# Kernel tuning notes

Hardware: AMD Instinct MI355X
Metric: run time of the kernel (lower is better)

The kernel has to match this reference:

```python
import math
import jax, jax.numpy as jnp
import numpy as np

B, IMG, P, D, DEPTH, NH, HD = 8, 384, 16, 768, 12, 12, 64
NREG, NS, NF = 4, 5, 16            # registers, special tokens (1 cls + 4 reg), rope freqs
HP = IMG // P                      # 24 patches per side
NPATCH = HP * HP                   # 576
ROPE_DIM = 2 * NF                  # 32
SCALE = HD ** -0.5


def setup_inputs() -> dict:
    key = jax.random.key(0)
    ks = jax.random.split(key, 12)
    s = 0.02
    rn = lambda k, shape: (jax.random.normal(k, shape, jnp.float32) * s)
    L, DF = DEPTH, 4 * D
    inp = {
        "pixel_values": jax.random.normal(ks[0], (B, 3, IMG, IMG), jnp.float32),
        "conv_w": rn(ks[1], (D, 3, P, P)),
        "conv_b": jnp.zeros((D,), jnp.float32),
        "cls_token": rn(ks[2], (1, 1, D)),
        "storage_tokens": rn(ks[3], (1, NREG, D)),
        "periods": jnp.exp(jnp.linspace(0.0, math.log(100.0), NF)).astype(jnp.float32),
        "ln1_s": jnp.ones((L, D), jnp.float32),
        "ln1_b": jnp.zeros((L, D), jnp.float32),
        "qkv_w": rn(ks[4], (L, 3 * D, D)),
        "qkv_b": rn(ks[5], (L, 3 * D)),
        "bias_mask": jnp.zeros((L, 3 * D), jnp.float32),  # buffer init zeros -> bias nulled
        "proj_w": rn(ks[6], (L, D, D)),
        "proj_b": jnp.zeros((L, D), jnp.float32),
        "ls1": jnp.ones((L, D), jnp.float32),
        "ln2_s": jnp.ones((L, D), jnp.float32),
        "ln2_b": jnp.zeros((L, D), jnp.float32),
        "fc1_w": rn(ks[7], (L, DF, D)),
        "fc1_b": jnp.zeros((L, DF), jnp.float32),
        "fc2_w": rn(ks[8], (L, D, DF)),
        "fc2_b": jnp.zeros((L, D), jnp.float32),
        "ls2": jnp.ones((L, D), jnp.float32),
        "lnf_s": jnp.ones((D,), jnp.float32),
        "lnf_b": jnp.zeros((D,), jnp.float32),
    }
    return inp


def _ln(x, s, b):
    mu = x.mean(-1, keepdims=True)
    var = ((x - mu) ** 2).mean(-1, keepdims=True)
    return (x - mu) / jnp.sqrt(var + 1e-6) * s + b


def _rot(x, cos, sin):
    # x: [b, h, n_patch, 2*NF]; cos/sin: [n_patch, NF]; interleaved even/odd rotation
    even, odd = x[..., 0::2], x[..., 1::2]
    return jnp.stack([even * cos - odd * sin, even * sin + odd * cos], axis=-1).reshape(x.shape)


def _forward(pixel_values, conv_w, conv_b, cls_token, storage_tokens, periods,
             ln1_s, ln1_b, qkv_w, qkv_b, bias_mask, proj_w, proj_b, ls1,
             ln2_s, ln2_b, fc1_w, fc1_b, fc2_w, fc2_b, ls2, lnf_s, lnf_b):
    b = pixel_values.shape[0]
    # Patch embed: stride == kernel conv as reshape + einsum
    xp = pixel_values.reshape(b, 3, HP, P, HP, P)
    tok = jnp.einsum('bchpwq,dcpq->bhwd', xp, conv_w) + conv_b       # [b,HP,HP,D]
    tok = tok.reshape(b, NPATCH, D)
    x = jnp.concatenate([jnp.broadcast_to(cls_token, (b, 1, D)),
                         jnp.broadcast_to(storage_tokens, (b, NREG, D)), tok], axis=1)
    n = x.shape[1]

    # RoPE tables (periods buffer; freqs = 2*pi / periods)
    freqs = (2.0 * math.pi) / periods                                 # [NF]
    pos = jnp.arange(HP, dtype=jnp.float32)
    gy, gx = jnp.meshgrid(pos, pos, indexing='ij')
    ax = gx.reshape(-1, 1) * freqs                                    # [NPATCH, NF]
    ay = gy.reshape(-1, 1) * freqs
    cos_x, sin_x = jnp.cos(ax), jnp.sin(ax)
    cos_y, sin_y = jnp.cos(ay), jnp.sin(ay)

    def blk(h, p):
        (l1s, l1b, qw, qb, bm, pw, pb, g1, l2s, l2b, f1w, f1b, f2w, f2b, g2) = p
        h1 = _ln(h, l1s, l1b)
        qkv = h1 @ qw.T + qb * bm                                     # bias nulled by mask
        qkv = qkv.reshape(b, n, 3, NH, HD).transpose(2, 0, 3, 1, 4)   # [3,b,NH,n,HD]
        q, k, v = qkv[0], qkv[1], qkv[2]
        # rotary on patch tokens; rope_total == HD so the whole head is rotated
        qp, kp = q[:, :, NS:], k[:, :, NS:]
        qp = jnp.concatenate([_rot(qp[..., :ROPE_DIM], cos_x, sin_x),
                              _rot(qp[..., ROPE_DIM:], cos_y, sin_y)], axis=-1)
        kp = jnp.concatenate([_rot(kp[..., :ROPE_DIM], cos_x, sin_x),
                              _rot(kp[..., ROPE_DIM:], cos_y, sin_y)], axis=-1)
        q = jnp.concatenate([q[:, :, :NS], qp], axis=2)
        k = jnp.concatenate([k[:, :, :NS], kp], axis=2)
        attn = jax.nn.softmax(jnp.einsum('bhqd,bhkd->bhqk', q, k) * SCALE, axis=-1)
        o = jnp.einsum('bhqk,bhkd->bhqd', attn, v).transpose(0, 2, 1, 3).reshape(b, n, D)
        h = h + g1 * (o @ pw.T + pb)
        h2 = _ln(h, l2s, l2b)
        m = jax.nn.gelu(h2 @ f1w.T + f1b, approximate=False) @ f2w.T + f2b
        h = h + g2 * m
        return h, None

    params = (ln1_s, ln1_b, qkv_w, qkv_b, bias_mask, proj_w, proj_b, ls1,
              ln2_s, ln2_b, fc1_w, fc1_b, fc2_w, fc2_b, ls2)
    x, _ = jax.lax.scan(blk, x, params)
    return _ln(x, lnf_s, lnf_b)


def reference(pixel_values, conv_w, conv_b, cls_token, storage_tokens, periods,
              ln1_s, ln1_b, qkv_w, qkv_b, bias_mask, proj_w, proj_b, ls1,
              ln2_s, ln2_b, fc1_w, fc1_b, fc2_w, fc2_b, ls2, lnf_s, lnf_b):
    return _forward(pixel_values, conv_w, conv_b, cls_token, storage_tokens, periods,
                    ln1_s, ln1_b, qkv_w, qkv_b, bias_mask, proj_w, proj_b, ls1,
                    ln2_s, ln2_b, fc1_w, fc1_b, fc2_w, fc2_b, ls2, lnf_s, lnf_b)
```

## Files before the change

### kernel.cpp

```cpp
#include <hip/hip_runtime.h>
#include <math.h>

typedef unsigned short u16;
typedef __attribute__((ext_vector_type(8))) short bf8;
typedef __attribute__((ext_vector_type(4))) float f4;

#define DEV static __device__ __forceinline__

DEV u16 f2b(float f){
  unsigned u = __builtin_bit_cast(unsigned, f);
  u += 0x7fffu + ((u >> 16) & 1u);
  return (u16)(u >> 16);
}
DEV float b2f(u16 h){
  unsigned u = ((unsigned)h) << 16;
  return __builtin_bit_cast(float, u);
}

#define BATCH  8
#define NTOK   581
#define NPAD   640
#define DIM    768
#define DFF    3072
#define NHEAD  12
#define HDIM   64
#define NLAYER 12
#define MTOK   (BATCH*NTOK)
#define MPAD2  4736
#define MCONV  (BATCH*576)
#define ATTN_SCALE 0.125f
#define BHEADS (BATCH*NHEAD)
#define QSZ    ((long long)BHEADS*NPAD*HDIM)

enum { EPI_CONV=0, EPI_QKV, EPI_PROJ, EPI_GELU, EPI_FC2 };

DEV int xcdswz(int lin, int n){
  int q = n >> 3, r = n & 7;
  int x = lin & 7, o = lin >> 3;
  return (x < r ? x*(q+1) : r*(q+1) + (x - r)*q) + o;
}

template<int EPI, int BM>
__global__ __launch_bounds__(256) void gemmRS(
    const u16* __restrict__ A, int lda,
    const u16* __restrict__ B, int ldb, int K,
    const float* __restrict__ bias,
    const float* __restrict__ aux,
    float* __restrict__ Cf,
    u16* __restrict__ Cb)
{
  constexpr int MR = BM / 32;
  const int gx = gridDim.x;
  const int lin = blockIdx.y * gx + blockIdx.x;
  const int tix = xcdswz(lin, gx * gridDim.y);
  const int bm = (tix / gx) * BM, bn = (tix % gx) * 64;
  __shared__ __attribute__((aligned(16))) u16 As[2][BM][40];
  __shared__ __attribute__((aligned(16))) u16 Bs[2][64][40];
  const int tid  = threadIdx.x;
  const int lane = tid & 63, wid = tid >> 6;
  const int wr = wid >> 1, wc = wid & 1;
  const int srow = tid >> 2, scol = (tid & 3) * 8;
  const u16* gA0 = A + (long long)(bm + srow) * lda + scol;
  const u16* gA1 = A + (long long)(bm + 64 + srow) * lda + scol;
  const u16* gB  = B + (long long)(bn + srow) * ldb + scol;
  const int frow = lane & 15, quad = lane >> 4, fk = quad * 8;

  f4 acc[MR][2] = {};
  const int T = K >> 5;

  auto compute = [&](int buf){
    bf8 af[MR], bf[2];
    #pragma unroll
    for (int m = 0; m < MR; ++m)
      af[m] = *(const bf8*)&As[buf][wr*(BM/2) + m*16 + frow][fk];
    #pragma unroll
    for (int n = 0; n < 2; ++n)
      bf[n] = *(const bf8*)&Bs[buf][wc*32 + n*16 + frow][fk];
    #pragma unroll
    for (int m = 0; m < MR; ++m)
    #pragma unroll
    for (int n = 0; n < 2; ++n)
      acc[m][n] = __builtin_amdgcn_mfma_f32_16x16x32_bf16(af[m], bf[n], acc[m][n], 0, 0, 0);
  };

  bf8 xA0, xA1, xB, yA0, yA1, yB;
  xA0 = *(const bf8*)gA0;        if constexpr (BM == 128) xA1 = *(const bf8*)gA1;
  xB  = *(const bf8*)gB;
  yA0 = *(const bf8*)(gA0 + 32); if constexpr (BM == 128) yA1 = *(const bf8*)(gA1 + 32);
  yB  = *(const bf8*)(gB + 32);
  *(bf8*)&As[0][srow][scol] = xA0;
  if constexpr (BM == 128) *(bf8*)&As[0][64 + srow][scol] = xA1;
  *(bf8*)&Bs[0][srow][scol] = xB;
  __syncthreads();

  for (int t = 0; t < T; t += 2){
    if (t + 2 < T){
      xA0 = *(const bf8*)(gA0 + (t+2)*32);
      if constexpr (BM == 128) xA1 = *(const bf8*)(gA1 + (t+2)*32);
      xB  = *(const bf8*)(gB  + (t+2)*32);
    }
    *(bf8*)&As[1][srow][scol] = yA0;
    if constexpr (BM == 128) *(bf8*)&As[1][64 + srow][scol] = yA1;
    *(bf8*)&Bs[1][srow][scol] = yB;
    compute(0);
    __syncthreads();
    if (t + 3 < T){
      yA0 = *(const bf8*)(gA0 + (t+3)*32);
      if constexpr (BM == 128) yA1 = *(const bf8*)(gA1 + (t+3)*32);
      yB  = *(const bf8*)(gB  + (t+3)*32);
    }
    if (t + 2 < T){
      *(bf8*)&As[0][srow][scol] = xA0;
      if constexpr (BM == 128) *(bf8*)&As[0][64 + srow][scol] = xA1;
      *(bf8*)&Bs[0][srow][scol] = xB;
    }
    compute(1);
    __syncthreads();
  }

  #pragma unroll
  for (int mi = 0; mi < MR; ++mi)
  #pragma unroll
  for (int ni = 0; ni < 2; ++ni){
    f4 v = acc[mi][ni];
    int col = bn + wc*32 + ni*16 + frow;
    int r0  = bm + wr*(BM/2) + mi*16 + quad*4;
    #pragma unroll
    for (int j = 0; j < 4; ++j){
      int m = r0 + j;
      float val = v[j];
      if constexpr (EPI == EPI_CONV){
        int b = m / 576, p = m % 576;
        Cf[((long long)b*NTOK + 5 + p)*DIM + col] = val + bias[col];
      } else if constexpr (EPI == EPI_QKV){
        if (m < MTOK){
          int b = m / NTOK, t = m % NTOK;
          int which = col / DIM, rem = col % DIM;
          int h = rem / HDIM, hd = rem % HDIM;
          float x = val + bias[col];
          long long bh = (long long)(b*NHEAD + h);
          if (which == 0) x *= ATTN_SCALE;
          if (which == 2)
            Cb[2*QSZ + (bh*HDIM + hd)*NPAD + t] = f2b(x);
          else
            Cb[(long long)which*QSZ + (bh*NPAD + t)*HDIM + hd] = f2b(x);
        }
      } else if constexpr (EPI == EPI_PROJ || EPI == EPI_FC2){
        if (m < MTOK)
          Cf[(long long)m*DIM + col] += aux[col] * (val + bias[col]);
      } else if constexpr (EPI == EPI_GELU){
        float x = val + bias[col];
        float g = 0.5f * x * (1.0f + erff(x * 0.70710678118f));
        Cb[(long long)m*DFF + col] = f2b(g);
      }
    }
  }
}

__global__ __launch_bounds__(256) void flash_k(
    const u16* __restrict__ Q, const u16* __restrict__ K,
    const u16* __restrict__ VT, u16* __restrict__ obuf)
{
  const int lid = blockIdx.x;
  const int xcd = lid & 7, slot = lid >> 3;
  const int bh = xcd * 12 + slot / 10;
  const int qb = slot % 10;
  const int b = bh / NHEAD, h = bh % NHEAD;
  const int tid = threadIdx.x, lane = tid & 63, w = tid >> 6;
  const int frow = lane & 15, quad = lane >> 4;
  __shared__ u16 P[4][16][80];
  const u16* Qb = Q  + (long long)bh * NPAD * HDIM;
  const u16* Kb = K  + (long long)bh * NPAD * HDIM;
  const u16* Vb = VT + (long long)bh * HDIM * NPAD;
  const bf8 qa0 = *(const bf8*)&Qb[(qb*64 + w*16 + frow)*HDIM + quad*8];
  const bf8 qa1 = *(const bf8*)&Qb[(qb*64 + w*16 + frow)*HDIM + 32 + quad*8];
  f4 o[4] = {};
  float m[4], l[4];
  #pragma unroll
  for (int j = 0; j < 4; ++j){ m[j] = -1e30f; l[j] = 0.0f; }

  bf8 kb0[4], kb1[4];
  #pragma unroll
  for (int n = 0; n < 4; ++n){
    const u16* kr = &Kb[(n*16 + frow)*HDIM + quad*8];
    kb0[n] = *(const bf8*)kr;
    kb1[n] = *(const bf8*)(kr + 32);
  }

  for (int kt = 0; kt < NPAD/64; ++kt){
    bf8 vb0[4], vb1[4];
    #pragma unroll
    for (int n = 0; n < 4; ++n){
      const u16* vr = &Vb[(n*16 + frow)*NPAD + kt*64 + quad*8];
      vb0[n] = *(const bf8*)vr;
      vb1[n] = *(const bf8*)(vr + 32);
    }
    f4 s[4];
    #pragma unroll
    for (int n = 0; n < 4; ++n){
      f4 z = {};
      z    = __builtin_amdgcn_mfma_f32_16x16x32_bf16(qa0, kb0[n], z, 0, 0, 0);
      s[n] = __builtin_amdgcn_mfma_f32_16x16x32_bf16(qa1, kb1[n], z, 0, 0, 0);
    }
    if (kt + 1 < NPAD/64){
      #pragma unroll
      for (int n = 0; n < 4; ++n){
        const u16* kr = &Kb[((kt+1)*64 + n*16 + frow)*HDIM + quad*8];
        kb0[n] = *(const bf8*)kr;
        kb1[n] = *(const bf8*)(kr + 32);
      }
    }
    if (kt == NPAD/64 - 1){
      #pragma unroll
      for (int n = 0; n < 4; ++n){
        int kcol = kt*64 + n*16 + frow;
        if (kcol >= NTOK){ s[n][0] = s[n][1] = s[n][2] = s[n][3] = -1e30f; }
      }
    }
    float sc[4];
    #pragma unroll
    for (int j = 0; j < 4; ++j){
      float v = fmaxf(fmaxf(s[0][j], s[1][j]), fmaxf(s[2][j], s[3][j]));
      v = fmaxf(v, __shfl_xor(v, 1));  v = fmaxf(v, __shfl_xor(v, 2));
      v = fmaxf(v, __shfl_xor(v, 4));  v = fmaxf(v, __shfl_xor(v, 8));
      float mn = fmaxf(m[j], v);
      sc[j] = __expf(m[j] - mn);
      m[j] = mn;
    }
    float ts[4] = {0.f, 0.f, 0.f, 0.f};
    #pragma unroll
    for (int n = 0; n < 4; ++n){
      #pragma unroll
      for (int j = 0; j < 4; ++j){
        float p = __expf(s[n][j] - m[j]);
        ts[j] += p;
        P[w][quad*4 + j][n*16 + frow] = f2b(p);
      }
    }
    #pragma unroll
    for (int j = 0; j < 4; ++j){
      float v = ts[j];
      v += __shfl_xor(v, 1); v += __shfl_xor(v, 2);
      v += __shfl_xor(v, 4); v += __shfl_xor(v, 8);
      l[j] = l[j]*sc[j] + v;
    }
    #pragma unroll
    for (int n = 0; n < 4; ++n)
    #pragma unroll
    for (int j = 0; j < 4; ++j) o[n][j] *= sc[j];
    bf8 pa0 = *(const bf8*)&P[w][frow][quad*8];
    bf8 pa1 = *(const bf8*)&P[w][frow][quad*8 + 32];
    #pragma unroll
    for (int n = 0; n < 4; ++n){
      o[n] = __builtin_amdgcn_mfma_f32_16x16x32_bf16(pa0, vb0[n], o[n], 0, 0, 0);
      o[n] = __builtin_amdgcn_mfma_f32_16x16x32_bf16(pa1, vb1[n], o[n], 0, 0, 0);
    }
  }
  #pragma unroll
  for (int j = 0; j < 4; ++j){
    int t = qb*64 + w*16 + quad*4 + j;
    if (t < NTOK){
      float inv = 1.0f / l[j];
      #pragma unroll
      for (int n = 0; n < 4; ++n)
        obuf[((long long)b*NTOK + t)*DIM + h*HDIM + n*16 + frow] = f2b(o[n][j] * inv);
    }
  }
}

template<int F32OUT>
__global__ __launch_bounds__(256) void ln_k(const float* __restrict__ x,
    const float* __restrict__ s, const float* __restrict__ b,
    u16* __restrict__ ob, float* __restrict__ of)
{
  const long long row = blockIdx.x;
  const float* xr = x + row * DIM;
  const int t = threadIdx.x;
  float v0 = xr[t], v1 = xr[t + 256], v2 = xr[t + 512];
  float sum = v0 + v1 + v2;
  #pragma unroll
  for (int o = 32; o; o >>= 1) sum += __shfl_down(sum, o);
  __shared__ float r1[4], r2[4];
  const int lane = t & 63, w = t >> 6;
  if (lane == 0) r1[w] = sum;
  __syncthreads();
  float mu = (r1[0] + r1[1] + r1[2] + r1[3]) * (1.0f / DIM);
  float d0 = v0 - mu, d1 = v1 - mu, d2 = v2 - mu;
  float vs = d0*d0 + d1*d1 + d2*d2;
  #pragma unroll
  for (int o = 32; o; o >>= 1) vs += __shfl_down(vs, o);
  if (lane == 0) r2[w] = vs;
  __syncthreads();
  float inv = 1.0f / sqrtf((r2[0] + r2[1] + r2[2] + r2[3]) * (1.0f / DIM) + 1e-6f);
  if constexpr (F32OUT){
    float* orow = of + row * DIM;
    orow[t]       = d0 * inv * s[t]       + b[t];
    orow[t + 256] = d1 * inv * s[t + 256] + b[t + 256];
    orow[t + 512] = d2 * inv * s[t + 512] + b[t + 512];
  } else {
    u16* orow = ob + row * DIM;
    orow[t]       = f2b(d0 * inv * s[t]       + b[t]);
    orow[t + 256] = f2b(d1 * inv * s[t + 256] + b[t + 256]);
    orow[t + 512] = f2b(d2 * inv * s[t + 512] + b[t + 512]);
  }
}

__global__ void ropetab_k(const float* __restrict__ periods, float* __restrict__ tab)
{
  int idx = blockIdx.x * blockDim.x + threadIdx.x;
  if (idx >= 24 * 16) return;
  int c = idx >> 4, f = idx & 15;
  float fr = 6.283185307179586f / periods[f];
  float a = (float)c * fr;
  tab[idx]       = cosf(a);
  tab[384 + idx] = sinf(a);
}

__global__ __launch_bounds__(256) void rope_k(u16* __restrict__ Q, u16* __restrict__ K,
                                              const float* __restrict__ tab)
{
  int idx = blockIdx.x * blockDim.x + threadIdx.x;
  if (idx >= BHEADS * 576 * 32) return;
  int f  = idx & 31;
  int p  = (idx >> 5) % 576;
  int bh = idx / (576 * 32);
  int px = p % 24, py = p / 24;
  float c, s; int d0;
  if (f < 16){ c = tab[px*16 + f];        s = tab[384 + px*16 + f];        d0 = 2*f; }
  else       { int ff = f - 16;
               c = tab[py*16 + ff];       s = tab[384 + py*16 + ff];       d0 = 32 + 2*ff; }
  long long off = (((long long)bh) * NPAD + 5 + p) * HDIM + d0;
  float qe = b2f(Q[off]), qo = b2f(Q[off + 1]);
  Q[off]     = f2b(qe * c - qo * s);
  Q[off + 1] = f2b(qe * s + qo * c);
  float ke = b2f(K[off]), ko = b2f(K[off + 1]);
  K[off]     = f2b(ke * c - ko * s);
  K[off + 1] = f2b(ke * s + ko * c);
}

__global__ void initx_k(float* __restrict__ x, const float* __restrict__ cls,
                        const float* __restrict__ stor)
{
  int idx = blockIdx.x * blockDim.x + threadIdx.x;
  if (idx >= BATCH * 5 * DIM) return;
  int d = idx % DIM; int t = (idx / DIM) % 5; int b = idx / (5 * DIM);
  x[((long long)b * NTOK + t) * DIM + d] = (t == 0) ? cls[d] : stor[(t - 1) * DIM + d];
}

__global__ void patch_k(const float* __restrict__ px, u16* __restrict__ Ap)
{
  int idx = blockIdx.x * blockDim.x + threadIdx.x;
  if (idx >= MCONV * DIM) return;
  int k = idx % DIM, m = idx / DIM;
  int b = m / 576, r = m % 576, hp = r / 24, wp = r % 24;
  int c = k / 256, rem = k % 256, p = rem / 16, q = rem % 16;
  float v = px[((((long long)b * 3 + c) * 384) + hp * 16 + p) * 384 + wp * 16 + q];
  Ap[idx] = f2b(v);
}

__global__ void cvt_k(const float* __restrict__ src, u16* __restrict__ dst, long long n)
{
  long long i = (long long)blockIdx.x * blockDim.x + threadIdx.x;
  long long stride = (long long)gridDim.x * blockDim.x;
  for (; i < n; i += stride) dst[i] = f2b(src[i]);
}

__global__ void biaseff_k(const float* __restrict__ qb, const float* __restrict__ bm,
                          float* __restrict__ out, int n)
{
  int i = blockIdx.x * blockDim.x + threadIdx.x;
  if (i < n) out[i] = qb[i] * bm[i];
}

extern "C" void kernel_launch(void* const* d_in, const int* in_sizes, int n_in,
                              void* d_out, int out_size, void* d_ws, size_t ws_size,
                              hipStream_t stream)
{
  const float* pixel   = (const float*)d_in[0];
  const float* conv_w  = (const float*)d_in[1];
  const float* conv_b  = (const float*)d_in[2];
  const float* cls     = (const float*)d_in[3];
  const float* stor    = (const float*)d_in[4];
  const float* periods = (const float*)d_in[5];
  const float* ln1s    = (const float*)d_in[6];
  const float* ln1b    = (const float*)d_in[7];
  const float* qkvw    = (const float*)d_in[8];
  const float* qkvb    = (const float*)d_in[9];
  const float* bmask   = (const float*)d_in[10];
  const float* projw   = (const float*)d_in[11];
  const float* projb   = (const float*)d_in[12];
  const float* ls1     = (const float*)d_in[13];
  const float* ln2s    = (const float*)d_in[14];
  const float* ln2b    = (const float*)d_in[15];
  const float* fc1w    = (const float*)d_in[16];
  const float* fc1b    = (const float*)d_in[17];
  const float* fc2w    = (const float*)d_in[18];
  const float* fc2b    = (const float*)d_in[19];
  const float* ls2     = (const float*)d_in[20];
  const float* lnfs    = (const float*)d_in[21];
  const float* lnfb    = (const float*)d_in[22];

  char* wsp = (char*)d_ws;
  auto alloc = [&](long long bytes) -> char* {
    char* p = wsp; wsp += (bytes + 255) & ~255LL; return p;
  };
  u16*   wqkv  = (u16*)  alloc((long long)NLAYER*2304*768*2);
  u16*   wproj = (u16*)  alloc((long long)NLAYER*768*768*2);
  u16*   wfc1  = (u16*)  alloc((long long)NLAYER*3072*768*2);
  u16*   wfc2  = (u16*)  alloc((long long)NLAYER*768*3072*2);
  u16*   wconv = (u16*)  alloc((long long)768*768*2);
  float* beff  = (float*)alloc((long long)NLAYER*2304*4);
  float* x     = (float*)alloc((long long)MPAD2*DIM*4);
  u16*   h     = (u16*)  alloc((long long)MPAD2*DIM*2);
  u16*   obuf  = (u16*)  alloc((long long)MPAD2*DIM*2);
  u16*   mlp   = (u16*)  alloc((long long)MPAD2*DFF*2);
  u16*   Ap    = (u16*)  alloc((long long)MCONV*DIM*2);
  u16*   Q     = (u16*)  alloc(QSZ*2*3);
  u16*   Kb    = Q + QSZ;
  u16*   VT    = Q + 2*QSZ;
  float* tab   = (float*)alloc((long long)2*24*16*4);
  if ((size_t)(wsp - (char*)d_ws) > ws_size) return;

  auto cvt = [&](const float* src, u16* dst, long long n){
    long long nb = (n + 255) / 256; if (nb > 4096) nb = 4096;
    cvt_k<<<(int)nb, 256, 0, stream>>>(src, dst, n);
  };
  cvt(qkvw,  wqkv,  (long long)NLAYER*2304*768);
  cvt(projw, wproj, (long long)NLAYER*768*768);
  cvt(fc1w,  wfc1,  (long long)NLAYER*3072*768);
  cvt(fc2w,  wfc2,  (long long)NLAYER*768*3072);
  cvt(conv_w, wconv, (long long)768*768);
  biaseff_k<<<(NLAYER*2304 + 255)/256, 256, 0, stream>>>(qkvb, bmask, beff, NLAYER*2304);
  ropetab_k<<<2, 256, 0, stream>>>(periods, tab);
  hipMemsetAsync(Q, 0, (size_t)QSZ*2*3, stream);

  patch_k<<<(MCONV*DIM + 255)/256, 256, 0, stream>>>(pixel, Ap);
  initx_k<<<(BATCH*5*DIM + 255)/256, 256, 0, stream>>>(x, cls, stor);
  gemmRS<EPI_CONV,64><<<dim3(DIM/64, MCONV/64), 256, 0, stream>>>(
      Ap, DIM, wconv, DIM, DIM, conv_b, nullptr, x, nullptr);

  for (int l = 0; l < NLAYER; ++l){
    ln_k<0><<<MTOK, 256, 0, stream>>>(x, ln1s + l*DIM, ln1b + l*DIM, h, nullptr);
    gemmRS<EPI_QKV,128><<<dim3(2304/64, MPAD2/128), 256, 0, stream>>>(
        h, DIM, wqkv + (long long)l*2304*768, DIM, DIM,
        beff + l*2304, nullptr, nullptr, Q);
    rope_k<<<(BHEADS*576*32 + 255)/256, 256, 0, stream>>>(Q, Kb, tab);
    flash_k<<<dim3(BHEADS*10), 256, 0, stream>>>(Q, Kb, VT, obuf);
    gemmRS<EPI_PROJ,64><<<dim3(DIM/64, MPAD2/64), 256, 0, stream>>>(
        obuf, DIM, wproj + (long long)l*768*768, DIM, DIM,
        projb + l*DIM, ls1 + l*DIM, x, nullptr);
    ln_k<0><<<MTOK, 256, 0, stream>>>(x, ln2s + l*DIM, ln2b + l*DIM, h, nullptr);
    gemmRS<EPI_GELU,128><<<dim3(DFF/64, MPAD2/128), 256, 0, stream>>>(
        h, DIM, wfc1 + (long long)l*3072*768, DIM, DIM,
        fc1b + l*DFF, nullptr, nullptr, mlp);
    gemmRS<EPI_FC2,64><<<dim3(DIM/64, MPAD2/64), 256, 0, stream>>>(
        mlp, DFF, wfc2 + (long long)l*768*3072, DFF, DFF,
        fc2b + l*DIM, ls2 + l*DIM, x, nullptr);
  }
  ln_k<1><<<MTOK, 256, 0, stream>>>(x, lnfs, lnfb, nullptr, (float*)d_out);
}
```

Before: 3.528 ms.

## Fuse RoPE into QKV epilogue and process two query blocks per flash block

Rotary embedding is now applied inside the QKV GEMM epilogue, where a lane-pair shuffle fetches the partner element. This removes the separate rope kernel and its read-modify-write pass over Q and K. The flash attention kernel now handles 128 query rows per block (two 64-row sub-blocks), so each K/V tile load is reused twice and the grid halves to 480 blocks. The shuffle assumes adjacent even/odd head dims sit in neighbouring lanes. Holding twice the accumulators raises register pressure, and the smaller grid may reduce occupancy.

```diff
diff --git a/kernel.cpp b/kernel.cpp
--- a/kernel.cpp
+++ b/kernel.cpp
@@ -134,16 +134,25 @@
         Cf[((long long)b*NTOK + 5 + p)*DIM + col] = val + bias[col];
       } else if constexpr (EPI == EPI_QKV){
         if (m < MTOK){
-          int b = m / NTOK, t = m % NTOK;
+          int b = m / NTOK, tt = m % NTOK;
           int which = col / DIM, rem = col % DIM;
           int h = rem / HDIM, hd = rem % HDIM;
           float x = val + bias[col];
+          if (which == 0) x *= ATTN_SCALE;
+          if (which < 2 && tt >= 5){
+            float po = __shfl_xor(x, 1);
+            int p = tt - 5;
+            int f = (hd & 31) >> 1;
+            int pc = (hd < 32) ? (p % 24) : (p / 24);
+            float c = aux[pc*16 + f];
+            float s = aux[384 + pc*16 + f];
+            x = (hd & 1) ? (po*s + x*c) : (x*c - po*s);
+          }
           long long bh = (long long)(b*NHEAD + h);
-          if (which == 0) x *= ATTN_SCALE;
           if (which == 2)
-            Cb[2*QSZ + (bh*HDIM + hd)*NPAD + t] = f2b(x);
+            Cb[2*QSZ + (bh*HDIM + hd)*NPAD + tt] = f2b(x);
           else
-            Cb[(long long)which*QSZ + (bh*NPAD + t)*HDIM + hd] = f2b(x);
+            Cb[(long long)which*QSZ + (bh*NPAD + tt)*HDIM + hd] = f2b(x);
         }
       } else if constexpr (EPI == EPI_PROJ || EPI == EPI_FC2){
         if (m < MTOK)
@@ -163,21 +172,28 @@
 {
   const int lid = blockIdx.x;
   const int xcd = lid & 7, slot = lid >> 3;
-  const int bh = xcd * 12 + slot / 10;
-  const int qb = slot % 10;
+  const int bh = xcd * 12 + slot / 5;
+  const int qb = slot % 5;
   const int b = bh / NHEAD, h = bh % NHEAD;
   const int tid = threadIdx.x, lane = tid & 63, w = tid >> 6;
   const int frow = lane & 15, quad = lane >> 4;
-  __shared__ u16 P[4][16][80];
+  __shared__ u16 P[4][2][16][80];
   const u16* Qb = Q  + (long long)bh * NPAD * HDIM;
   const u16* Kb = K  + (long long)bh * NPAD * HDIM;
   const u16* Vb = VT + (long long)bh * HDIM * NPAD;
-  const bf8 qa0 = *(const bf8*)&Qb[(qb*64 + w*16 + frow)*HDIM + quad*8];
-  const bf8 qa1 = *(const bf8*)&Qb[(qb*64 + w*16 + frow)*HDIM + 32 + quad*8];
-  f4 o[4] = {};
-  float m[4], l[4];
-  #pragma unroll
-  for (int j = 0; j < 4; ++j){ m[j] = -1e30f; l[j] = 0.0f; }
+  bf8 qa0[2], qa1[2];
+  #pragma unroll
+  for (int bd = 0; bd < 2; ++bd){
+    const u16* qr = &Qb[(qb*128 + bd*64 + w*16 + frow)*HDIM + quad*8];
+    qa0[bd] = *(const bf8*)qr;
+    qa1[bd] = *(const bf8*)(qr + 32);
+  }
+  f4 o[2][4] = {};
+  float m[2][4], l[2][4];
+  #pragma unroll
+  for (int bd = 0; bd < 2; ++bd)
+  #pragma unroll
+  for (int j = 0; j < 4; ++j){ m[bd][j] = -1e30f; l[bd][j] = 0.0f; }
 
   bf8 kb0[4], kb1[4];
   #pragma unroll
@@ -195,12 +211,14 @@
       vb0[n] = *(const bf8*)vr;
       vb1[n] = *(const bf8*)(vr + 32);
     }
-    f4 s[4];
-    #pragma unroll
-    for (int n = 0; n < 4; ++n){
+    f4 s[2][4];
+    #pragma unroll
+    for (int n = 0; n < 4; ++n)
+    #pragma unroll
+    for (int bd = 0; bd < 2; ++bd){
       f4 z = {};
-      z    = __builtin_amdgcn_mfma_f32_16x16x32_bf16(qa0, kb0[n], z, 0, 0, 0);
-      s[n] = __builtin_amdgcn_mfma_f32_16x16x32_bf16(qa1, kb1[n], z, 0, 0, 0);
+      z        = __builtin_amdgcn_mfma_f32_16x16x32_bf16(qa0[bd], kb0[n], z, 0, 0, 0);
+      s[bd][n] = __builtin_amdgcn_mfma_f32_16x16x32_bf16(qa1[bd], kb1[n], z, 0, 0, 0);
     }
     if (kt + 1 < NPAD/64){
       #pragma unroll
@@ -214,56 +232,65 @@
       #pragma unroll
       for (int n = 0; n < 4; ++n){
         int kcol = kt*64 + n*16 + frow;
-        if (kcol >= NTOK){ s[n][0] = s[n][1] = s[n][2] = s[n][3] = -1e30f; }
-      }
-    }
-    float sc[4];
-    #pragma unroll
-    for (int j = 0; j < 4; ++j){
-      float v = fmaxf(fmaxf(s[0][j], s[1][j]), fmaxf(s[2][j], s[3][j]));
-      v = fmaxf(v, __shfl_xor(v, 1));  v = fmaxf(v, __shfl_xor(v, 2));
-      v = fmaxf(v, __shfl_xor(v, 4));  v = fmaxf(v, __shfl_xor(v, 8));
-      float mn = fmaxf(m[j], v);
-      sc[j] = __expf(m[j] - mn);
-      m[j] = mn;
-    }
-    float ts[4] = {0.f, 0.f, 0.f, 0.f};
-    #pragma unroll
-    for (int n = 0; n < 4; ++n){
+        if (kcol >= NTOK){
+          #pragma unroll
+          for (int bd = 0; bd < 2; ++bd)
+            s[bd][n][0] = s[bd][n][1] = s[bd][n][2] = s[bd][n][3] = -1e30f;
+        }
+      }
+    }
+    #pragma unroll
+    for (int bd = 0; bd < 2; ++bd){
+      float sc[4];
       #pragma unroll
       for (int j = 0; j < 4; ++j){
-        float p = __expf(s[n][j] - m[j]);
-        ts[j] += p;
-        P[w][quad*4 + j][n*16 + frow] = f2b(p);
-      }
-    }
-    #pragma unroll
-    for (int j = 0; j < 4; ++j){
-      float v = ts[j];
-      v += __shfl_xor(v, 1); v += __shfl_xor(v, 2);
-      v += __shfl_xor(v, 4); v += __shfl_xor(v, 8);
-      l[j] = l[j]*sc[j] + v;
-    }
-    #pragma unroll
-    for (int n = 0; n < 4; ++n)
-    #pragma unroll
-    for (int j = 0; j < 4; ++j) o[n][j] *= sc[j];
-    bf8 pa0 = *(const bf8*)&P[w][frow][quad*8];
-    bf8 pa1 = *(const bf8*)&P[w][frow][quad*8 + 32];
-    #pragma unroll
-    for (int n = 0; n < 4; ++n){
-      o[n] = __builtin_amdgcn_mfma_f32_16x16x32_bf16(pa0, vb0[n], o[n], 0, 0, 0);
-      o[n] = __builtin_amdgcn_mfma_f32_16x16x32_bf16(pa1, vb1[n], o[n], 0, 0, 0);
-    }
-  }
+        float v = fmaxf(fmaxf(s[bd][0][j], s[bd][1][j]), fmaxf(s[bd][2][j], s[bd][3][j]));
+        v = fmaxf(v, __shfl_xor(v, 1));  v = fmaxf(v, __shfl_xor(v, 2));
+        v = fmaxf(v, __shfl_xor(v, 4));  v = fmaxf(v, __shfl_xor(v, 8));
+        float mn = fmaxf(m[bd][j], v);
+        sc[j] = __expf(m[bd][j] - mn);
+        m[bd][j] = mn;
+      }
+      float ts[4] = {0.f, 0.f, 0.f, 0.f};
+      #pragma unroll
+      for (int n = 0; n < 4; ++n){
+        #pragma unroll
+        for (int j = 0; j < 4; ++j){
+          float p = __expf(s[bd][n][j] - m[bd][j]);
+          ts[j] += p;
+          P[w][bd][quad*4 + j][n*16 + frow] = f2b(p);
+        }
+      }
+      #pragma unroll
+      for (int j = 0; j < 4; ++j){
+        float v = ts[j];
+        v += __shfl_xor(v, 1); v += __shfl_xor(v, 2);
+        v += __shfl_xor(v, 4); v += __shfl_xor(v, 8);
+        l[bd][j] = l[bd][j]*sc[j] + v;
+      }
+      #pragma unroll
+      for (int n = 0; n < 4; ++n)
+      #pragma unroll
+      for (int j = 0; j < 4; ++j) o[bd][n][j] *= sc[j];
+      bf8 pa0 = *(const bf8*)&P[w][bd][frow][quad*8];
+      bf8 pa1 = *(const bf8*)&P[w][bd][frow][quad*8 + 32];
+      #pragma unroll
+      for (int n = 0; n < 4; ++n){
+        o[bd][n] = __builtin_amdgcn_mfma_f32_16x16x32_bf16(pa0, vb0[n], o[bd][n], 0, 0, 0);
+        o[bd][n] = __builtin_amdgcn_mfma_f32_16x16x32_bf16(pa1, vb1[n], o[bd][n], 0, 0, 0);
+      }
+    }
+  }
+  #pragma unroll
+  for (int bd = 0; bd < 2; ++bd)
   #pragma unroll
   for (int j = 0; j < 4; ++j){
-    int t = qb*64 + w*16 + quad*4 + j;
+    int t = qb*128 + bd*64 + w*16 + quad*4 + j;
     if (t < NTOK){
-      float inv = 1.0f / l[j];
+      float inv = 1.0f / l[bd][j];
       #pragma unroll
       for (int n = 0; n < 4; ++n)
-        obuf[((long long)b*NTOK + t)*DIM + h*HDIM + n*16 + frow] = f2b(o[n][j] * inv);
+        obuf[((long long)b*NTOK + t)*DIM + h*HDIM + n*16 + frow] = f2b(o[bd][n][j] * inv);
     }
   }
 }
@@ -314,28 +341,6 @@
   float a = (float)c * fr;
   tab[idx]       = cosf(a);
   tab[384 + idx] = sinf(a);
-}
-
-__global__ __launch_bounds__(256) void rope_k(u16* __restrict__ Q, u16* __restrict__ K,
-                                              const float* __restrict__ tab)
-{
-  int idx = blockIdx.x * blockDim.x + threadIdx.x;
-  if (idx >= BHEADS * 576 * 32) return;
-  int f  = idx & 31;
-  int p  = (idx >> 5) % 576;
-  int bh = idx / (576 * 32);
-  int px = p % 24, py = p / 24;
-  float c, s; int d0;
-  if (f < 16){ c = tab[px*16 + f];        s = tab[384 + px*16 + f];        d0 = 2*f; }
-  else       { int ff = f - 16;
-               c = tab[py*16 + ff];       s = tab[384 + py*16 + ff];       d0 = 32 + 2*ff; }
-  long long off = (((long long)bh) * NPAD + 5 + p) * HDIM + d0;
-  float qe = b2f(Q[off]), qo = b2f(Q[off + 1]);
-  Q[off]     = f2b(qe * c - qo * s);
-  Q[off + 1] = f2b(qe * s + qo * c);
-  float ke = b2f(K[off]), ko = b2f(K[off + 1]);
-  K[off]     = f2b(ke * c - ko * s);
-  K[off + 1] = f2b(ke * s + ko * c);
 }
 
 __global__ void initx_k(float* __restrict__ x, const float* __restrict__ cls,
@@ -443,9 +448,8 @@
     ln_k<0><<<MTOK, 256, 0, stream>>>(x, ln1s + l*DIM, ln1b + l*DIM, h, nullptr);
     gemmRS<EPI_QKV,128><<<dim3(2304/64, MPAD2/128), 256, 0, stream>>>(
         h, DIM, wqkv + (long long)l*2304*768, DIM, DIM,
-        beff + l*2304, nullptr, nullptr, Q);
-    rope_k<<<(BHEADS*576*32 + 255)/256, 256, 0, stream>>>(Q, Kb, tab);
-    flash_k<<<dim3(BHEADS*10), 256, 0, stream>>>(Q, Kb, VT, obuf);
+        beff + l*2304, tab, nullptr, Q);
+    flash_k<<<dim3(480), 256, 0, stream>>>(Q, Kb, VT, obuf);
     gemmRS<EPI_PROJ,64><<<dim3(DIM/64, MPAD2/64), 256, 0, stream>>>(
         obuf, DIM, wproj + (long long)l*768*768, DIM, DIM,
         projb + l*DIM, ls1 + l*DIM, x, nullptr);
```

New measurement: 3.173 ms. -10.1%, faster.
